# Optimization experiments

Measured on AMD Instinct MI355X. Metric: run time of the kernel, lower is better.

Reference implementation:

```python
import jax, jax.numpy as jnp
import numpy as np
from jax import lax

HEADS = 8
DIM_HEAD = 64
MODALITIES = 8
QUERY_DIM = 128
INNER = HEADS * DIM_HEAD  # 512


def _conv(x, w):
    # x: (b, Cin, H, W), w: (Cout, Cin, kh, kw), VALID padding (padding done manually)
    return lax.conv_general_dilated(x, w, window_strides=(1, 1), padding='VALID',
                                    dimension_numbers=('NCHW', 'OIHW', 'NCHW'))


def _reflect_pad_w(x):
    # ReflectionPad2d((2,2,0,0)): pad width (last) axis by 2 on each side
    return jnp.pad(x, ((0, 0), (0, 0), (0, 0), (2, 2)), mode='reflect')


def setup_inputs() -> dict:
    key = jax.random.key(0)
    k1, k2, k3, k4 = jax.random.split(key, 4)
    b, n, m, c = 2, 4096, MODALITIES, QUERY_DIM
    x = jax.random.normal(k1, (b, n, m, c), dtype=jnp.float32)
    Wq = jax.random.normal(k2, (INNER, c, 1, 5), dtype=jnp.float32) * 0.02
    Wkv = jax.random.normal(k3, (2 * INNER, c, 1, 5), dtype=jnp.float32) * 0.02
    Wout = jax.random.normal(k4, (c * m, INNER, m, 5), dtype=jnp.float32) * 0.02
    return {"x": x, "Wq": Wq, "Wkv": Wkv, "Wout": Wout}


def reference(x, Wq, Wkv, Wout):
    b, n, m, c = x.shape
    h, d = HEADS, DIM_HEAD
    scale = d ** -0.5

    xp = _reflect_pad_w(jnp.transpose(x, (0, 3, 2, 1)))  # (b, c, m, n+4)
    q = _conv(xp, Wq)                                     # (b, h*d, m, n)
    kv = _conv(xp, Wkv)                                   # (b, 2*h*d, m, n)
    k, v = kv[:, :h * d], kv[:, h * d:]

    # channel axis (h d) split: h outer, d inner -> (b, h, d, m, n)
    q = q.reshape(b, h, d, m, n)
    k = k.reshape(b, h, d, m, n)
    v = v.reshape(b, h, d, m, n)

    # attention over sequence axis n; feature dim is (m d) per head
    sim = jnp.einsum('bhdmi,bhdmj->bhij', q, k) * scale   # (b, h, n, n)
    attn = jax.nn.softmax(sim, axis=-1)
    out = jnp.einsum('bhij,bhdmj->bhdmi', attn, v)        # (b, h, d, m, n)

    out = out.reshape(b, h * d, m, n)                     # 'b (h d) m n'
    o = _conv(_reflect_pad_w(out), Wout)                  # (b, c*m, 1, n)
    o = o.reshape(b, c, m, 1, n)[:, :, :, 0, :]           # squeeze height-1 dim -> (b, c, m, n)
    return o.reshape(x.shape)                             # torch .view(x_shape) is a raw reshape
```

## Files before the change

kernel.cpp:

```cpp
#include <hip/hip_runtime.h>
#include <stdint.h>


typedef __attribute__((ext_vector_type(8))) short short8;
typedef __attribute__((ext_vector_type(4))) short short4v;
typedef __attribute__((ext_vector_type(2))) short short2v;
typedef __attribute__((ext_vector_type(4))) float f32x4;
typedef __attribute__((ext_vector_type(16))) float f32x16;

__device__ __forceinline__ f32x4 mfma16(short8 a, short8 b, f32x4 c) {
  return __builtin_amdgcn_mfma_f32_16x16x32_bf16(a, b, c, 0, 0, 0);
}
__device__ __forceinline__ f32x16 mfma32(short8 a, short8 b, f32x16 c) {
  return __builtin_amdgcn_mfma_f32_32x32x16_bf16(a, b, c, 0, 0, 0);
}

__device__ __forceinline__ unsigned short f2bf(float f) {
  union { float f; uint32_t u; } v; v.f = f;
  uint32_t r = (v.u + 0x7fffu + ((v.u >> 16) & 1u)) >> 16;
  return (unsigned short)r;
}

__device__ __forceinline__ uint32_t cvtpk(float lo, float hi) {
  uint32_t r;
  asm volatile("v_cvt_pk_bf16_f32 %0, %1, %2" : "=v"(r) : "v"(lo), "v"(hi));
  return r;
}
__device__ __forceinline__ void plswap(uint32_t& a, uint32_t& b) {
  asm volatile("v_permlane32_swap_b32 %0, %1" : "+v"(a), "+v"(b));
}

__device__ __forceinline__ int refl4096(int p) {
  p = p < 0 ? -p : p;
  return p >= 4096 ? 8190 - p : p;
}

__device__ __forceinline__ void gl_lds16(const void* g, void* l) {
  __builtin_amdgcn_global_load_lds(
      (const __attribute__((address_space(1))) void*)g,
      (__attribute__((address_space(3))) void*)l, 16, 0, 0);
}

__global__ void k_convw_qkv(const float* __restrict__ Wq,
                            const float* __restrict__ Wkv,
                            unsigned short* __restrict__ out) {
  int e = blockIdx.x * 256 + threadIdx.x;
  int oc = e / 640, k = e - oc * 640;
  int ci = k & 127, t = k >> 7;
  float w = (oc < 512) ? Wq[oc * 640 + ci * 5 + t]
                       : Wkv[(oc - 512) * 640 + ci * 5 + t];
  out[e] = f2bf(w);
}

__global__ __launch_bounds__(256)
void k_convx(const float* __restrict__ x, unsigned short* __restrict__ xb,
             int b) {
  int e = (blockIdx.x * 256 + threadIdx.x) * 8;
  const float* src = x + (size_t)b * 4194304 + e;
  f32x4 v0 = *(const f32x4*)src;
  f32x4 v1 = *(const f32x4*)(src + 4);
  short8 pk;
  pk[0] = (short)f2bf(v0[0]); pk[1] = (short)f2bf(v0[1]);
  pk[2] = (short)f2bf(v0[2]); pk[3] = (short)f2bf(v0[3]);
  pk[4] = (short)f2bf(v1[0]); pk[5] = (short)f2bf(v1[1]);
  pk[6] = (short)f2bf(v1[2]); pk[7] = (short)f2bf(v1[3]);
  *(short8*)(xb + e) = pk;
}

__global__ __launch_bounds__(256)
void k_convw_out(const float* __restrict__ Wout,
                 unsigned short* __restrict__ out) {
  __shared__ unsigned short row_l[20480];
  const int oc = blockIdx.x;
  const int tid = threadIdx.x;
  const float* src = Wout + (size_t)oc * 20480;
#pragma unroll
  for (int i0 = 0; i0 < 5120; i0 += 256) {
    int i = i0 + tid;
    f32x4 v = *(const f32x4*)(src + (size_t)i * 4);
    short4v pk;
    pk[0] = (short)f2bf(v[0]); pk[1] = (short)f2bf(v[1]);
    pk[2] = (short)f2bf(v[2]); pk[3] = (short)f2bf(v[3]);
    *(short4v*)(row_l + i * 4) = pk;
  }
  __syncthreads();
  unsigned short* drow = out + (size_t)oc * 20480;
#pragma unroll
  for (int r0 = 0; r0 < 20480; r0 += 512) {
    int e = r0 + tid * 2;
    int t0 = e >> 12, ft0 = e & 4095;
    int t1 = (e + 1) >> 12, ft1 = (e + 1) & 4095;
    short2v pk;
    pk[0] = (short)row_l[(ft0 >> 3) * 40 + (ft0 & 7) * 5 + t0];
    pk[1] = (short)row_l[(ft1 >> 3) * 40 + (ft1 & 7) * 5 + t1];
    *(short2v*)(drow + e) = pk;
  }
}

__global__ __launch_bounds__(256, 2)
void k_qkv(const unsigned short* __restrict__ xb,
           const unsigned short* __restrict__ Wb,
           unsigned short* __restrict__ Qg, unsigned short* __restrict__ Kg,
           unsigned short* __restrict__ Vg) {
  __shared__ __align__(16) unsigned short As[128 * 64];
  __shared__ __align__(16) unsigned short Bs[128 * 64];
  const int tid = threadIdx.x;
  const int lane = tid & 63, w = tid >> 6;
  const int wr = w >> 1, wc = w & 1;
  const int l15 = lane & 15, lg = lane >> 4;
  const int p0 = blockIdx.x * 128;
  const int ocb = blockIdx.y * 128;
  const int m = blockIdx.z;

  f32x4 acc[4][4];
#pragma unroll
  for (int i = 0; i < 4; i++)
#pragma unroll
    for (int j = 0; j < 4; j++) acc[i][j] = (f32x4){0.f, 0.f, 0.f, 0.f};

  for (int ks = 0; ks < 10; ks++) {
    const int t = ks >> 1;
    const int ci0 = (ks & 1) << 6;
    __syncthreads();
#pragma unroll
    for (int i = 0; i < 4; i++) {
      int s = tid + (i << 8);
      int row = s >> 3, c = s & 7;
      int cs = c ^ (row & 7);
      int xn = refl4096(p0 + row - 2 + t);
      gl_lds16(xb + (((size_t)xn << 3) + m) * 128 + ci0 + (cs << 3),
               (char*)As + (size_t)s * 16);
    }
#pragma unroll
    for (int c = 0; c < 4; c++) {
      int sb = ((c << 2) + w) << 6;
      int slot = sb + lane;
      int row = slot >> 3, cc = slot & 7;
      int cs = cc ^ (row & 7);
      gl_lds16(Wb + (size_t)(ocb + row) * 640 + (ks << 6) + (cs << 3),
               (char*)Bs + (size_t)sb * 16);
    }
    __syncthreads();
#pragma unroll
    for (int kk = 0; kk < 2; kk++) {
      short8 af[4], bq[4];
#pragma unroll
      for (int i = 0; i < 4; i++) {
        int row = (wr << 6) + (i << 4) + l15;
        af[i] = *(const short8*)((char*)As + (row << 7) +
                                 ((((kk << 2) + lg) ^ (row & 7)) << 4));
      }
#pragma unroll
      for (int j = 0; j < 4; j++) {
        int row = (wc << 6) + (j << 4) + l15;
        bq[j] = *(const short8*)((char*)Bs + (row << 7) +
                                 ((((kk << 2) + lg) ^ (row & 7)) << 4));
      }
#pragma unroll
      for (int i = 0; i < 4; i++)
#pragma unroll
        for (int j = 0; j < 4; j++) acc[i][j] = mfma16(af[i], bq[j], acc[i][j]);
    }
  }

  const int region = ocb >> 9;
  const float QSCALE = 0.18033688f;
#pragma unroll
  for (int i = 0; i < 4; i++) {
    const int posb = p0 + (wr << 6) + (i << 4) + (lg << 2);
#pragma unroll
    for (int j = 0; j < 4; j++) {
      const int oc = ocb + (wc << 6) + (j << 4) + l15;
      const int ocr = oc & 511;
      const int hh = ocr >> 6, dd = ocr & 63;
      const int f = (dd << 3) + m;
      if (region == 0) {
        size_t base = (size_t)hh * 4096 * 512 + f;
#pragma unroll
        for (int r = 0; r < 4; r++)
          Qg[base + (size_t)(posb + r) * 512] = f2bf(acc[i][j][r] * QSCALE);
      } else if (region == 1) {
        size_t base = (size_t)hh * 4096 * 512 + f;
#pragma unroll
        for (int r = 0; r < 4; r++)
          Kg[base + (size_t)(posb + r) * 512] = f2bf(acc[i][j][r]);
      } else {
        short4v pk;
#pragma unroll
        for (int r = 0; r < 4; r++) pk[r] = (short)f2bf(acc[i][j][r]);
        *(short4v*)(Vg + ((size_t)hh * 512 + f) * 4096 + posb) = pk;
      }
    }
  }
}

__global__ __launch_bounds__(512, 2)
void k_attn(const unsigned short* __restrict__ Qg,
            const unsigned short* __restrict__ Kg,
            const unsigned short* __restrict__ Vg,
            unsigned short* __restrict__ AO) {
  __shared__ __align__(16) char lds[131584];
  char* Kt = lds;
  char* Vt0 = lds + 32768;
  char* Vt1 = lds + 65536;
  char* Sx = lds + 98304;
  float* Ls = (float*)(lds + 131072);

  const int tid = threadIdx.x;
  const int lane = tid & 63, w = tid >> 6;
  const int l31 = lane & 31, hi = lane >> 5;
  const int wpair = w >> 1, whalf = w & 1;
  const int h = blockIdx.x & 7;
  const int qblk = blockIdx.x >> 3;
  const int qbase = qblk * 128 + wpair * 32;
  const int fh = whalf << 8;

  const size_t kb = (size_t)h * 4096 * 512;
  const size_t vb = (size_t)h * 512 * 4096;

  short8 q[16];
  {
    const unsigned short* qp =
        Qg + ((size_t)h * 4096 + qbase + l31) * 512 + fh + hi * 8;
#pragma unroll
    for (int ks = 0; ks < 16; ks++) q[ks] = *(const short8*)(qp + ks * 16);
  }

  f32x16 o[8];
#pragma unroll
  for (int t = 0; t < 8; t++)
#pragma unroll
    for (int e = 0; e < 16; e++) o[t][e] = 0.f;
  float lacc = 0.f;

  const int rb = l31 >> 1;
  const int swz = rb & 7;
  const int cg0 = ((l31 & 1) << 2) + hi;
  const int voff1 = rb * 128 + ((cg0 ^ swz) << 4);
  const int voff2 = rb * 128 + (((cg0 + 2) ^ swz) << 4);

  char* sxw = Sx + (w << 10) + (lane << 4);
  char* sxp = Sx + ((w ^ 1) << 10) + (lane << 4);

  union U { uint32_t d[4]; short8 s; };

  auto stageK = [&](int it) {
    const int key0 = it << 5;
#pragma unroll
    for (int i = 0; i < 4; i++) {
      int s = tid + (i << 9);
      int r = s >> 6, c = s & 63;
      gl_lds16(Kg + kb + (size_t)(key0 + r) * 512 + ((c ^ r) << 3),
               Kt + (size_t)s * 16);
    }
  };
  auto stageV = [&](int it, char* Vt) {
    const int key0 = it << 5;
#pragma unroll
    for (int i = 0; i < 4; i++) {
      int s = tid + (i << 9);
      int rp = s >> 3, c = s & 7;
      int cu = c ^ (rp & 7);
      int f = (rp << 1) + (cu >> 2);
      gl_lds16(Vg + vb + (size_t)f * 4096 + key0 + ((cu & 3) << 3),
               Vt + (size_t)s * 16);
    }
  };

  stageK(0);
  stageV(0, Vt0);

  for (int it = 0; it < 128; it++) {
    char* Vt = (it & 1) ? Vt1 : Vt0;
    char* Vn = (it & 1) ? Vt0 : Vt1;
    __syncthreads();

    if (it < 127) stageV(it + 1, Vn);

    f32x16 st;
#pragma unroll
    for (int e = 0; e < 16; e++) st[e] = 0.f;
#pragma unroll
    for (int ks = 0; ks < 16; ks++) {
      int ch = ((fh >> 3) + (ks << 1) + hi) ^ l31;
      short8 kfrag = *(const short8*)(Kt + (l31 << 10) + (ch << 4));
      st = mfma32(kfrag, q[ks], st);
    }
#pragma unroll
    for (int j = 0; j < 4; j++) {
      f32x4 pw = (f32x4){st[4 * j], st[4 * j + 1], st[4 * j + 2], st[4 * j + 3]};
      *(f32x4*)(sxw + (j << 13)) = pw;
    }
    __syncthreads();

    if (it < 127) stageK(it + 1);

#pragma unroll
    for (int j = 0; j < 4; j++) {
      f32x4 pv = *(const f32x4*)(sxp + (j << 13));
      st[4 * j] += pv[0]; st[4 * j + 1] += pv[1];
      st[4 * j + 2] += pv[2]; st[4 * j + 3] += pv[3];
    }

    float p[16];
#pragma unroll
    for (int r = 0; r < 16; r++) p[r] = __builtin_amdgcn_exp2f(st[r]);
    lacc += ((p[0] + p[1]) + (p[2] + p[3])) + ((p[4] + p[5]) + (p[6] + p[7])) +
            (((p[8] + p[9]) + (p[10] + p[11])) +
             ((p[12] + p[13]) + (p[14] + p[15])));

    uint32_t d0 = cvtpk(p[0], p[1]),  d1 = cvtpk(p[2], p[3]);
    uint32_t d2 = cvtpk(p[4], p[5]),  d3 = cvtpk(p[6], p[7]);
    uint32_t d4 = cvtpk(p[8], p[9]),  d5 = cvtpk(p[10], p[11]);
    uint32_t d6 = cvtpk(p[12], p[13]), d7 = cvtpk(p[14], p[15]);
    plswap(d0, d2); plswap(d1, d3);
    plswap(d4, d6); plswap(d5, d7);
    U u1; u1.d[0] = d0; u1.d[1] = d1; u1.d[2] = d2; u1.d[3] = d3;
    U u2; u2.d[0] = d4; u2.d[1] = d5; u2.d[2] = d6; u2.d[3] = d7;

#pragma unroll
    for (int tt = 0; tt < 8; tt++) {
      const char* vrow = Vt + (((whalf << 3) + tt) << 11);
      short8 v1 = *(const short8*)(vrow + voff1);
      short8 v2 = *(const short8*)(vrow + voff2);
      o[tt] = mfma32(u1.s, v1, o[tt]);
      o[tt] = mfma32(u2.s, v2, o[tt]);
    }
  }

  lacc += __shfl_xor(lacc, 32, 64);
  if (whalf == 0) Ls[(wpair << 5) + l31] = lacc;
  __syncthreads();

  float linv[16];
#pragma unroll
  for (int r = 0; r < 16; r++) {
    int qq = (r & 3) + ((r >> 2) << 3) + (hi << 2);
    linv[r] = 1.f / Ls[(wpair << 5) + qq];
  }
#pragma unroll
  for (int tt = 0; tt < 8; tt++) {
    size_t col = (size_t)h * 512 + (((whalf << 3) + tt) << 5) + l31;
#pragma unroll
    for (int r = 0; r < 16; r++) {
      int qq = qbase + (r & 3) + ((r >> 2) << 3) + (hi << 2);
      AO[(size_t)qq * 4096 + col] = f2bf(o[tt][r] * linv[r]);
    }
  }
}

__global__ __launch_bounds__(512, 2)
void k_outconv(const unsigned short* __restrict__ AO,
               const unsigned short* __restrict__ WB,
               float* __restrict__ outp, int b) {
  __shared__ __align__(16) unsigned short As[2][8192];
  __shared__ __align__(16) unsigned short Bs[2][8192];
  const int tid = threadIdx.x;
  const int lane = tid & 63, w = tid >> 6;
  const int wr = w >> 1, wc = w & 1;
  const int l15 = lane & 15, lg = lane >> 4;
  const int i0 = (blockIdx.x >> 3) * 128;
  const int ocb = (blockIdx.x & 7) * 128;

  f32x4 acc[2][4];
#pragma unroll
  for (int i = 0; i < 2; i++)
#pragma unroll
    for (int j = 0; j < 4; j++) acc[i][j] = (f32x4){0.f, 0.f, 0.f, 0.f};

  auto stage = [&](int ks, int d) {
    const int t = ks >> 6;
    const int f0 = (ks & 63) << 6;
    const int k0 = ks << 6;
#pragma unroll
    for (int i = 0; i < 2; i++) {
      int s = tid + (i << 9);
      int row = s >> 3, c = s & 7;
      int cs = c ^ (row & 7);
      int sr = refl4096(i0 + row + t - 2);
      gl_lds16(AO + (size_t)sr * 4096 + f0 + (cs << 3),
               (char*)As[d] + (size_t)s * 16);
    }
#pragma unroll
    for (int i = 0; i < 2; i++) {
      int s = tid + (i << 9);
      int row = s >> 3, c = s & 7;
      int cs = c ^ (row & 7);
      gl_lds16(WB + (size_t)(ocb + row) * 20480 + k0 + (cs << 3),
               (char*)Bs[d] + (size_t)s * 16);
    }
  };

  stage(0, 0);

  for (int ks = 0; ks < 320; ks++) {
    const int d = ks & 1;
    __syncthreads();
    if (ks < 319) stage(ks + 1, d ^ 1);
#pragma unroll
    for (int kk = 0; kk < 2; kk++) {
      short8 af[2], bq[4];
#pragma unroll
      for (int i = 0; i < 2; i++) {
        int row = (wr << 5) + (i << 4) + l15;
        af[i] = *(const short8*)((char*)As[d] + (row << 7) +
                                 ((((kk << 2) + lg) ^ (row & 7)) << 4));
      }
#pragma unroll
      for (int j = 0; j < 4; j++) {
        int row = (wc << 6) + (j << 4) + l15;
        bq[j] = *(const short8*)((char*)Bs[d] + (row << 7) +
                                 ((((kk << 2) + lg) ^ (row & 7)) << 4));
      }
#pragma unroll
      for (int i = 0; i < 2; i++)
#pragma unroll
        for (int j = 0; j < 4; j++) acc[i][j] = mfma16(af[i], bq[j], acc[i][j]);
    }
  }
#pragma unroll
  for (int i = 0; i < 2; i++)
#pragma unroll
    for (int j = 0; j < 4; j++) {
      int oc = ocb + (wc << 6) + (j << 4) + l15;
      int pos = i0 + (wr << 5) + (i << 4) + (lg << 2);
      *(f32x4*)(outp + ((size_t)b * 1024 + oc) * 4096 + pos) = acc[i][j];
    }
}

extern "C" void kernel_launch(void* const* d_in, const int* in_sizes, int n_in,
                              void* d_out, int out_size, void* d_ws,
                              size_t ws_size, hipStream_t stream) {
  const float* x = (const float*)d_in[0];
  const float* Wq = (const float*)d_in[1];
  const float* Wkv = (const float*)d_in[2];
  const float* Wout = (const float*)d_in[3];
  float* out = (float*)d_out;
  char* ws = (char*)d_ws;

  const size_t SEG = 33554432;
  unsigned short* Qg = (unsigned short*)ws;
  unsigned short* Kg = (unsigned short*)(ws + SEG);
  unsigned short* Vg = (unsigned short*)(ws + 2 * SEG);
  unsigned short* AO = (unsigned short*)(ws + 3 * SEG);
  unsigned short* xb = AO;
  unsigned short* WB1 = (unsigned short*)(ws + 4 * SEG);
  unsigned short* WB2 = (unsigned short*)ws;

  k_convw_qkv<<<3840, 256, 0, stream>>>(Wq, Wkv, WB1);
  for (int b = 0; b < 2; b++) {
    k_convx<<<2048, 256, 0, stream>>>(x, xb, b);
    k_qkv<<<dim3(32, 12, 8), 256, 0, stream>>>(xb, WB1, Qg, Kg, Vg);
    k_attn<<<256, 512, 0, stream>>>(Qg, Kg, Vg, AO);
    k_convw_out<<<1024, 256, 0, stream>>>(Wout, WB2);
    k_outconv<<<256, 512, 0, stream>>>(AO, WB2, out, b);
  }
}
```

Baseline: 1.624 ms.

## Load V and out-conv weights directly from global, drop their LDS staging

In the attention kernel, V fragments are now read straight from global memory per lane instead of being staged through double-buffered LDS. K gets the freed LDS as a double buffer, and its prefetch moves to the start of each iteration. In the output conv kernel, weight fragments are read directly from global into registers each k-step and the B LDS buffer is removed. This cuts LDS footprint and staging traffic, but global latency is now exposed on the MFMA path, with no prefetch ahead and less coalesced V/W access.

```diff
diff --git a/kernel.cpp b/kernel.cpp
--- a/kernel.cpp
+++ b/kernel.cpp
@@ -199,12 +199,11 @@
             const unsigned short* __restrict__ Kg,
             const unsigned short* __restrict__ Vg,
             unsigned short* __restrict__ AO) {
-  __shared__ __align__(16) char lds[131584];
-  char* Kt = lds;
-  char* Vt0 = lds + 32768;
-  char* Vt1 = lds + 65536;
-  char* Sx = lds + 98304;
-  float* Ls = (float*)(lds + 131072);
+  __shared__ __align__(16) char lds[98816];
+  char* Kt0 = lds;
+  char* Kt1 = lds + 32768;
+  char* Sx = lds + 65536;
+  float* Ls = (float*)(lds + 98304);
 
   const int tid = threadIdx.x;
   const int lane = tid & 63, w = tid >> 6;
@@ -233,18 +232,15 @@
     for (int e = 0; e < 16; e++) o[t][e] = 0.f;
   float lacc = 0.f;
 
-  const int rb = l31 >> 1;
-  const int swz = rb & 7;
-  const int cg0 = ((l31 & 1) << 2) + hi;
-  const int voff1 = rb * 128 + ((cg0 ^ swz) << 4);
-  const int voff2 = rb * 128 + (((cg0 + 2) ^ swz) << 4);
+  const unsigned short* vlane =
+      Vg + vb + (size_t)((whalf << 8) + l31) * 4096 + (hi << 3);
 
   char* sxw = Sx + (w << 10) + (lane << 4);
   char* sxp = Sx + ((w ^ 1) << 10) + (lane << 4);
 
   union U { uint32_t d[4]; short8 s; };
 
-  auto stageK = [&](int it) {
+  auto stageK = [&](int it, char* Kt) {
     const int key0 = it << 5;
 #pragma unroll
     for (int i = 0; i < 4; i++) {
@@ -254,28 +250,16 @@
                Kt + (size_t)s * 16);
     }
   };
-  auto stageV = [&](int it, char* Vt) {
+
+  stageK(0, Kt0);
+
+  for (int it = 0; it < 128; it++) {
     const int key0 = it << 5;
-#pragma unroll
-    for (int i = 0; i < 4; i++) {
-      int s = tid + (i << 9);
-      int rp = s >> 3, c = s & 7;
-      int cu = c ^ (rp & 7);
-      int f = (rp << 1) + (cu >> 2);
-      gl_lds16(Vg + vb + (size_t)f * 4096 + key0 + ((cu & 3) << 3),
-               Vt + (size_t)s * 16);
-    }
-  };
-
-  stageK(0);
-  stageV(0, Vt0);
-
-  for (int it = 0; it < 128; it++) {
-    char* Vt = (it & 1) ? Vt1 : Vt0;
-    char* Vn = (it & 1) ? Vt0 : Vt1;
+    char* Ktc = (it & 1) ? Kt1 : Kt0;
+    char* Ktn = (it & 1) ? Kt0 : Kt1;
     __syncthreads();
 
-    if (it < 127) stageV(it + 1, Vn);
+    if (it < 127) stageK(it + 1, Ktn);
 
     f32x16 st;
 #pragma unroll
@@ -283,7 +267,7 @@
 #pragma unroll
     for (int ks = 0; ks < 16; ks++) {
       int ch = ((fh >> 3) + (ks << 1) + hi) ^ l31;
-      short8 kfrag = *(const short8*)(Kt + (l31 << 10) + (ch << 4));
+      short8 kfrag = *(const short8*)(Ktc + (l31 << 10) + (ch << 4));
       st = mfma32(kfrag, q[ks], st);
     }
 #pragma unroll
@@ -292,8 +276,6 @@
       *(f32x4*)(sxw + (j << 13)) = pw;
     }
     __syncthreads();
-
-    if (it < 127) stageK(it + 1);
 
 #pragma unroll
     for (int j = 0; j < 4; j++) {
@@ -318,11 +300,11 @@
     U u1; u1.d[0] = d0; u1.d[1] = d1; u1.d[2] = d2; u1.d[3] = d3;
     U u2; u2.d[0] = d4; u2.d[1] = d5; u2.d[2] = d6; u2.d[3] = d7;
 
+    const unsigned short* vp = vlane + key0;
 #pragma unroll
     for (int tt = 0; tt < 8; tt++) {
-      const char* vrow = Vt + (((whalf << 3) + tt) << 11);
-      short8 v1 = *(const short8*)(vrow + voff1);
-      short8 v2 = *(const short8*)(vrow + voff2);
+      short8 v1 = *(const short8*)(vp + (size_t)tt * 131072);
+      short8 v2 = *(const short8*)(vp + (size_t)tt * 131072 + 16);
       o[tt] = mfma32(u1.s, v1, o[tt]);
       o[tt] = mfma32(u2.s, v2, o[tt]);
     }
@@ -354,7 +336,6 @@
                const unsigned short* __restrict__ WB,
                float* __restrict__ outp, int b) {
   __shared__ __align__(16) unsigned short As[2][8192];
-  __shared__ __align__(16) unsigned short Bs[2][8192];
   const int tid = threadIdx.x;
   const int lane = tid & 63, w = tid >> 6;
   const int wr = w >> 1, wc = w & 1;
@@ -368,10 +349,18 @@
 #pragma unroll
     for (int j = 0; j < 4; j++) acc[i][j] = (f32x4){0.f, 0.f, 0.f, 0.f};
 
-  auto stage = [&](int ks, int d) {
+  const unsigned short* wbase[2][4];
+#pragma unroll
+  for (int kk = 0; kk < 2; kk++)
+#pragma unroll
+    for (int j = 0; j < 4; j++)
+      wbase[kk][j] = WB +
+          (size_t)(ocb + (wc << 6) + (j << 4) + l15) * 20480 +
+          (kk << 5) + (lg << 3);
+
+  auto stageA = [&](int ks, int d) {
     const int t = ks >> 6;
     const int f0 = (ks & 63) << 6;
-    const int k0 = ks << 6;
 #pragma unroll
     for (int i = 0; i < 2; i++) {
       int s = tid + (i << 9);
@@ -381,25 +370,27 @@
       gl_lds16(AO + (size_t)sr * 4096 + f0 + (cs << 3),
                (char*)As[d] + (size_t)s * 16);
     }
-#pragma unroll
-    for (int i = 0; i < 2; i++) {
-      int s = tid + (i << 9);
-      int row = s >> 3, c = s & 7;
-      int cs = c ^ (row & 7);
-      gl_lds16(WB + (size_t)(ocb + row) * 20480 + k0 + (cs << 3),
-               (char*)Bs[d] + (size_t)s * 16);
-    }
   };
 
-  stage(0, 0);
+  stageA(0, 0);
 
   for (int ks = 0; ks < 320; ks++) {
     const int d = ks & 1;
+    const int k0 = ks << 6;
     __syncthreads();
-    if (ks < 319) stage(ks + 1, d ^ 1);
+
+    short8 wf[2][4];
+#pragma unroll
+    for (int kk = 0; kk < 2; kk++)
+#pragma unroll
+      for (int j = 0; j < 4; j++)
+        wf[kk][j] = *(const short8*)(wbase[kk][j] + k0);
+
+    if (ks < 319) stageA(ks + 1, d ^ 1);
+
 #pragma unroll
     for (int kk = 0; kk < 2; kk++) {
-      short8 af[2], bq[4];
+      short8 af[2];
 #pragma unroll
       for (int i = 0; i < 2; i++) {
         int row = (wr << 5) + (i << 4) + l15;
@@ -407,15 +398,10 @@
                                  ((((kk << 2) + lg) ^ (row & 7)) << 4));
       }
 #pragma unroll
-      for (int j = 0; j < 4; j++) {
-        int row = (wc << 6) + (j << 4) + l15;
-        bq[j] = *(const short8*)((char*)Bs[d] + (row << 7) +
-                                 ((((kk << 2) + lg) ^ (row & 7)) << 4));
-      }
-#pragma unroll
       for (int i = 0; i < 2; i++)
 #pragma unroll
-        for (int j = 0; j < 4; j++) acc[i][j] = mfma16(af[i], bq[j], acc[i][j]);
+        for (int j = 0; j < 4; j++)
+          acc[i][j] = mfma16(af[i], wf[kk][j], acc[i][j]);
     }
   }
 #pragma unroll
```

Result: slower. 3.034 ms (+86.8%).
